# Performance work log

Hardware: AMD Instinct MI355X
Metric: run time of the kernel (lower is better)

## Reference

```python
import jax, jax.numpy as jnp
import numpy as np

B, N, E, D, R, M, L = 8, 8192, 16384, 128, 200, 20, 3


def setup_inputs() -> dict:
    key = jax.random.key(0)
    ks = jax.random.split(key, 16)
    return {
        "dists": jax.random.randint(ks[0], (B, N), 0, 10),
        "edge_index": jax.random.randint(ks[1], (B, 2, E), 0, N),
        "rels": jax.random.randint(ks[2], (B, E), 0, R),
        "node_mask": jax.random.randint(ks[3], (B, N), 0, 2).astype(bool),
        "edge_mask": jax.random.randint(ks[4], (B, E), 0, 2).astype(bool),
        "r_query_embed": jax.random.normal(ks[5], (B, D), dtype=jnp.float32),
        "conf_embeds": jax.random.normal(ks[6], (B, E, D), dtype=jnp.float32),
        "noise": jax.random.normal(ks[7], (B, N, D), dtype=jnp.float32),
        "dist_table": jax.random.normal(ks[8], (10, D), dtype=jnp.float32) * 0.02,
        "rel_table": jax.random.normal(ks[9], (R, D), dtype=jnp.float32) * 0.02,
        "msg_W": jax.random.normal(ks[10], (L, 5 * D, D), dtype=jnp.float32) / np.sqrt(5 * D),
        "msg_b": jnp.zeros((L, D), jnp.float32),
        "upd_W": jax.random.normal(ks[11], (L, D, D), dtype=jnp.float32) / np.sqrt(D),
        "upd_b": jnp.zeros((L, D), jnp.float32),
        "att_W": jax.random.normal(ks[12], (2 * D, 1), dtype=jnp.float32) / np.sqrt(2 * D),
        "att_b": jnp.zeros((1,), jnp.float32),
    }


def reference(dists, edge_index, rels, node_mask, edge_mask, r_query_embed,
              conf_embeds, noise, dist_table, rel_table, msg_W, msg_b,
              upd_W, upd_b, att_W, att_b):
    dist_emb = dist_table[jnp.clip(dists, 0, 9)]            # [B,N,D]
    h = dist_emb + noise * 0.1
    src = edge_index[:, 0, :]                               # [B,E]
    tgt = edge_index[:, 1, :]                               # [B,E]
    em = edge_mask[..., None].astype(h.dtype)               # [B,E,1]
    h_r = rel_table[rels]                                   # [B,E,D]
    dist_src = jnp.take_along_axis(dist_emb, src[..., None], axis=1)  # [B,E,D]

    def scatter_add(t_idx, msg):
        return jnp.zeros((N, D), msg.dtype).at[t_idx].add(msg)

    for k in range(L):
        h_src = jnp.take_along_axis(h, src[..., None], axis=1)        # [B,E,D]
        comp = h_src * h_r
        msg_in = jnp.concatenate([comp, h_src, dist_src, h_r, conf_embeds], axis=-1)  # [B,E,5D]
        msg = jax.nn.relu(jnp.einsum('bef,fd->bed', msg_in, msg_W[k]) + msg_b[k]) * em
        aggr = jax.vmap(scatter_add)(tgt, msg)                        # [B,N,D]
        h = jnp.einsum('bnd,df->bnf', aggr, upd_W[k]) + upd_b[k] + h

    h = h * node_mask[..., None].astype(h.dtype)
    t_state = h[:, 0, :]
    r_q = jnp.broadcast_to(r_query_embed[:, None, :], (B, N, D))
    att_in = jnp.concatenate([h, r_q], axis=-1)                       # [B,N,2D]
    scores = jax.nn.leaky_relu((att_in @ att_W + att_b)[..., 0], 0.01)
    scores = jnp.where(node_mask, scores, -1e9)
    alpha = jax.nn.softmax(scores, axis=1)
    topk_vals, topk_idx = jax.lax.top_k(alpha, M)                     # [B,M]
    H_evd = jnp.take_along_axis(h, topk_idx[..., None], axis=1) * topk_vals[..., None]
    return (H_evd, t_state)
```

## Files before the change

### kernel.cpp

```cpp
#include <hip/hip_runtime.h>
#include <hip/hip_bf16.h>
#include <math.h>

#define B_ 8
#define N_ 8192
#define E_ 16384
#define D_ 128
#define R_ 200
#define M_ 20
#define L_ 3
#define KEFF 384

typedef __attribute__((ext_vector_type(8))) short bf16x8;
typedef __attribute__((ext_vector_type(4))) float f32x4;

__device__ __forceinline__ short f2b(float f) {
  union { __hip_bfloat16 b; short s; } u;
  u.b = __float2bfloat16(f);
  return u.s;
}

__global__ __launch_bounds__(256) void k_init_h(const int* __restrict__ dists,
    const float* __restrict__ noise, const float* __restrict__ dist_table,
    float* __restrict__ h) {
  int i = blockIdx.x * 256 + threadIdx.x;
  int row = i >> 5;
  int d4 = i & 31;
  int dc = dists[row]; dc = dc < 0 ? 0 : (dc > 9 ? 9 : dc);
  const float4 t = *(const float4*)&dist_table[dc * D_ + d4 * 4];
  const float4 nz = *(const float4*)&noise[(size_t)i * 4];
  float4 o;
  o.x = t.x + 0.1f * nz.x; o.y = t.y + 0.1f * nz.y;
  o.z = t.z + 0.1f * nz.z; o.w = t.w + 0.1f * nz.w;
  *(float4*)&h[(size_t)i * 4] = o;
}

__global__ __launch_bounds__(256) void k_compact(const int* __restrict__ edge_mask,
    int* __restrict__ count, int* __restrict__ list) {
  int i = blockIdx.x * 256 + threadIdx.x;
  bool act = edge_mask[i] != 0;
  unsigned long long m = __ballot(act);
  int lane = threadIdx.x & 63;
  int base = 0;
  if (lane == 0) base = atomicAdd(count, __popcll(m));
  base = __shfl(base, 0);
  if (act) list[base + __popcll(m & ((1ull << lane) - 1ull))] = i;
}

__global__ __launch_bounds__(128) void k_tables(const float* __restrict__ dist_table,
    const float* __restrict__ rel_table, const float* __restrict__ msg_W,
    const float* __restrict__ msg_b, float* __restrict__ T3b, float* __restrict__ T4) {
  int k = blockIdx.x / 210;
  int r = blockIdx.x % 210;
  int d = threadIdx.x;
  if (r < 10) {
    float acc = msg_b[k * D_ + d];
    for (int f = 0; f < D_; ++f)
      acc = fmaf(dist_table[r * D_ + f], msg_W[(size_t)(k * 640 + 256 + f) * D_ + d], acc);
    T3b[(k * 10 + r) * D_ + d] = acc;
  } else {
    int rr = r - 10;
    float acc = 0.f;
    for (int f = 0; f < D_; ++f)
      acc = fmaf(rel_table[rr * D_ + f], msg_W[(size_t)(k * 640 + 384 + f) * D_ + d], acc);
    T4[(k * R_ + rr) * D_ + d] = acc;
  }
}

__global__ __launch_bounds__(256) void k_wbt_msg(const float* __restrict__ msg_W,
    short* __restrict__ Wbt) {
  int idx = blockIdx.x * 256 + threadIdx.x;
  int fe = idx % KEFF;
  int t = idx / KEFF;
  int n = t & 127;
  int k = t >> 7;
  int row = fe < 256 ? fe : fe + 256;
  Wbt[idx] = f2b(msg_W[(size_t)(k * 640 + row) * D_ + n]);
}

__global__ __launch_bounds__(256) void k_wbt_upd(const float* __restrict__ upd_W,
    short* __restrict__ Wbt) {
  int idx = blockIdx.x * 256 + threadIdx.x;
  int f = idx & 127;
  int t = idx >> 7;
  int n = t & 127;
  int k = t >> 7;
  Wbt[idx] = f2b(upd_W[(size_t)(k * D_ + f) * D_ + n]);
}

__global__ __launch_bounds__(256) void k_msg(
    const int* __restrict__ count_p, const int* __restrict__ list,
    const int* __restrict__ edge_index, const int* __restrict__ rels,
    const int* __restrict__ dists, const float* __restrict__ h,
    const float* __restrict__ rel_table, const float* __restrict__ conf,
    const short* __restrict__ Wbt,
    const float* __restrict__ T3b,
    const float* __restrict__ T4,
    float* __restrict__ aggr) {
  int cnt = *count_p;
  int base = blockIdx.x * 64;
  if (base >= cnt) return;
  int ne = min(64, cnt - base);
  __shared__ __align__(16) short sA[64][72];
  __shared__ __align__(16) short sB[128][72];
  __shared__ int sMeta[64][5];
  int tid = threadIdx.x;
  if (tid < 64) {
    if (tid < ne) {
      int id = list[base + tid];
      int b = id >> 14;
      int e = id & (E_ - 1);
      int src = edge_index[(b * 2) * E_ + e];
      int tgt = edge_index[(b * 2 + 1) * E_ + e];
      int dc = dists[b * N_ + src];
      dc = dc < 0 ? 0 : (dc > 9 ? 9 : dc);
      sMeta[tid][0] = b * N_ + src;
      sMeta[tid][1] = id;
      sMeta[tid][2] = b * N_ + tgt;
      sMeta[tid][3] = dc;
      sMeta[tid][4] = rels[id];
    } else {
      sMeta[tid][0] = 0; sMeta[tid][1] = 0; sMeta[tid][2] = 0;
      sMeta[tid][3] = 0; sMeta[tid][4] = 0;
    }
  }
  __syncthreads();
  int lane = tid & 63, wv = tid >> 6;
  int wm = wv >> 1, wn = wv & 1;
  int g = lane >> 4, cl = lane & 15;
  f32x4 acc[2][4];
  f32x4 zz = {0.f, 0.f, 0.f, 0.f};
#pragma unroll
  for (int tm = 0; tm < 2; ++tm)
#pragma unroll
    for (int tn = 0; tn < 4; ++tn) acc[tm][tn] = zz;
  int si = tid >> 2, sq = tid & 3;
  int nB = tid >> 1, hB = tid & 1;
  for (int kc = 0; kc < 6; ++kc) {
    float v[16];
    if (si < ne) {
      int c0 = kc * 64 + sq * 16;
      if (kc < 2) {
        const float4* hp = (const float4*)&h[(size_t)sMeta[si][0] * D_ + c0];
        const float4* rp = (const float4*)&rel_table[sMeta[si][4] * D_ + c0];
#pragma unroll
        for (int j = 0; j < 4; ++j) {
          float4 a = hp[j], r = rp[j];
          v[4*j] = a.x*r.x; v[4*j+1] = a.y*r.y; v[4*j+2] = a.z*r.z; v[4*j+3] = a.w*r.w;
        }
      } else if (kc < 4) {
        const float4* hp = (const float4*)&h[(size_t)sMeta[si][0] * D_ + (c0 - 128)];
#pragma unroll
        for (int j = 0; j < 4; ++j) {
          float4 a = hp[j];
          v[4*j] = a.x; v[4*j+1] = a.y; v[4*j+2] = a.z; v[4*j+3] = a.w;
        }
      } else {
        const float4* cp = (const float4*)&conf[(size_t)sMeta[si][1] * D_ + (c0 - 256)];
#pragma unroll
        for (int j = 0; j < 4; ++j) {
          float4 a = cp[j];
          v[4*j] = a.x; v[4*j+1] = a.y; v[4*j+2] = a.z; v[4*j+3] = a.w;
        }
      }
    } else {
#pragma unroll
      for (int j = 0; j < 16; ++j) v[j] = 0.f;
    }
    bf16x8 p0, p1;
#pragma unroll
    for (int j = 0; j < 8; ++j) { p0[j] = f2b(v[j]); p1[j] = f2b(v[j + 8]); }
    *(bf16x8*)&sA[si][sq * 16] = p0;
    *(bf16x8*)&sA[si][sq * 16 + 8] = p1;
    const bf16x8* wp = (const bf16x8*)&Wbt[(size_t)nB * KEFF + kc * 64 + hB * 32];
#pragma unroll
    for (int j = 0; j < 4; ++j) *(bf16x8*)&sB[nB][hB * 32 + j * 8] = wp[j];
    __syncthreads();
#pragma unroll
    for (int ks = 0; ks < 2; ++ks) {
      int co = ks * 32 + g * 8;
      bf16x8 af[2], bfr[4];
      af[0] = *(const bf16x8*)&sA[wm * 32 + cl][co];
      af[1] = *(const bf16x8*)&sA[wm * 32 + 16 + cl][co];
#pragma unroll
      for (int tn = 0; tn < 4; ++tn)
        bfr[tn] = *(const bf16x8*)&sB[wn * 64 + tn * 16 + cl][co];
#pragma unroll
      for (int tm = 0; tm < 2; ++tm)
#pragma unroll
        for (int tn = 0; tn < 4; ++tn)
          acc[tm][tn] = __builtin_amdgcn_mfma_f32_16x16x32_bf16(af[tm], bfr[tn], acc[tm][tn], 0, 0, 0);
    }
    __syncthreads();
  }
#pragma unroll
  for (int tm = 0; tm < 2; ++tm)
#pragma unroll
    for (int reg = 0; reg < 4; ++reg) {
      int edge = wm * 32 + tm * 16 + g * 4 + reg;
      if (edge < ne) {
        int arow = sMeta[edge][2];
        int dc = sMeta[edge][3];
        int rl = sMeta[edge][4];
#pragma unroll
        for (int tn = 0; tn < 4; ++tn) {
          int n = wn * 64 + tn * 16 + cl;
          float bias = T3b[dc * D_ + n] + T4[rl * D_ + n];
          float vv = fmaxf(acc[tm][tn][reg] + bias, 0.f);
          unsafeAtomicAdd(&aggr[(size_t)arow * D_ + n], vv);
        }
      }
    }
}

__global__ __launch_bounds__(256) void k_upd(
    float* __restrict__ aggr, const short* __restrict__ Wbt,
    const float* __restrict__ upd_b, float* __restrict__ h) {
  int base = blockIdx.x * 64;
  __shared__ __align__(16) short sA[64][72];
  __shared__ __align__(16) short sB[128][72];
  int tid = threadIdx.x;
  int lane = tid & 63, wv = tid >> 6;
  int wm = wv >> 1, wn = wv & 1;
  int g = lane >> 4, cl = lane & 15;
  f32x4 acc[2][4];
  f32x4 zz = {0.f, 0.f, 0.f, 0.f};
#pragma unroll
  for (int tm = 0; tm < 2; ++tm)
#pragma unroll
    for (int tn = 0; tn < 4; ++tn) acc[tm][tn] = zz;
  int si = tid >> 2, sq = tid & 3;
  int nB = tid >> 1, hB = tid & 1;
  for (int kc = 0; kc < 2; ++kc) {
    float4* ap = (float4*)&aggr[(size_t)(base + si) * D_ + kc * 64 + sq * 16];
    float v[16];
    float4 z4 = make_float4(0.f, 0.f, 0.f, 0.f);
#pragma unroll
    for (int j = 0; j < 4; ++j) {
      float4 a = ap[j];
      ap[j] = z4;
      v[4*j] = a.x; v[4*j+1] = a.y; v[4*j+2] = a.z; v[4*j+3] = a.w;
    }
    bf16x8 p0, p1;
#pragma unroll
    for (int j = 0; j < 8; ++j) { p0[j] = f2b(v[j]); p1[j] = f2b(v[j + 8]); }
    *(bf16x8*)&sA[si][sq * 16] = p0;
    *(bf16x8*)&sA[si][sq * 16 + 8] = p1;
    const bf16x8* wp = (const bf16x8*)&Wbt[(size_t)nB * D_ + kc * 64 + hB * 32];
#pragma unroll
    for (int j = 0; j < 4; ++j) *(bf16x8*)&sB[nB][hB * 32 + j * 8] = wp[j];
    __syncthreads();
#pragma unroll
    for (int ks = 0; ks < 2; ++ks) {
      int co = ks * 32 + g * 8;
      bf16x8 af[2], bfr[4];
      af[0] = *(const bf16x8*)&sA[wm * 32 + cl][co];
      af[1] = *(const bf16x8*)&sA[wm * 32 + 16 + cl][co];
#pragma unroll
      for (int tn = 0; tn < 4; ++tn)
        bfr[tn] = *(const bf16x8*)&sB[wn * 64 + tn * 16 + cl][co];
#pragma unroll
      for (int tm = 0; tm < 2; ++tm)
#pragma unroll
        for (int tn = 0; tn < 4; ++tn)
          acc[tm][tn] = __builtin_amdgcn_mfma_f32_16x16x32_bf16(af[tm], bfr[tn], acc[tm][tn], 0, 0, 0);
    }
    __syncthreads();
  }
#pragma unroll
  for (int tm = 0; tm < 2; ++tm)
#pragma unroll
    for (int reg = 0; reg < 4; ++reg) {
      int grow = base + wm * 32 + tm * 16 + g * 4 + reg;
#pragma unroll
      for (int tn = 0; tn < 4; ++tn) {
        int n = wn * 64 + tn * 16 + cl;
        size_t gi = (size_t)grow * D_ + n;
        h[gi] = acc[tm][tn][reg] + upd_b[n] + h[gi];
      }
    }
}

__global__ __launch_bounds__(256) void k_score(const float* __restrict__ h,
    const int* __restrict__ node_mask, const float* __restrict__ r_query,
    const float* __restrict__ att_W, const float* __restrict__ att_b,
    float* __restrict__ sSg) {
  int wv = threadIdx.x >> 6, lane = threadIdx.x & 63;
  int node = blockIdx.x * 4 + wv;
  int b = node >> 13;
  float s;
  if (node_mask[node] == 0) {
    s = -1e9f;
  } else {
    float2 hv = *(const float2*)&h[(size_t)node * D_ + lane * 2];
    float2 w0 = *(const float2*)&att_W[lane * 2];
    float2 w1 = *(const float2*)&att_W[D_ + lane * 2];
    float2 rq = *(const float2*)&r_query[b * D_ + lane * 2];
    float v = hv.x * w0.x + hv.y * w0.y + rq.x * w1.x + rq.y * w1.y;
#pragma unroll
    for (int off = 32; off > 0; off >>= 1) v += __shfl_xor(v, off);
    v += att_b[0];
    s = v > 0.f ? v : 0.01f * v;
  }
  if (lane == 0) sSg[node] = s;
}

__global__ __launch_bounds__(1024) void k_top(const float* __restrict__ sSg,
    const float* __restrict__ h, const int* __restrict__ node_mask,
    float* __restrict__ out) {
  int b = blockIdx.x;
  int tid = threadIdx.x, lane = tid & 63, wv = tid >> 6;
  __shared__ float sS[N_];
  __shared__ float sRw[16];
  __shared__ float sSegV[16];
  __shared__ int sSegI[16];
  __shared__ float sTopV[M_];
  __shared__ int sTopI[M_];
  __shared__ float sMax, sSum;
  const float4* gp = (const float4*)&sSg[(size_t)b * N_];
#pragma unroll
  for (int r = 0; r < 2; ++r) {
    float4 x = gp[tid + r * 1024];
    *(float4*)&sS[(tid + r * 1024) * 4] = x;
  }
  __syncthreads();
  float lm = -INFINITY;
  for (int n = tid; n < N_; n += 1024) lm = fmaxf(lm, sS[n]);
#pragma unroll
  for (int off = 32; off > 0; off >>= 1) lm = fmaxf(lm, __shfl_xor(lm, off));
  if (lane == 0) sRw[wv] = lm;
  __syncthreads();
  if (tid == 0) {
    float m = sRw[0];
    for (int i = 1; i < 16; ++i) m = fmaxf(m, sRw[i]);
    sMax = m;
  }
  __syncthreads();
  float mx = sMax;
  float ls = 0.f;
  for (int n = tid; n < N_; n += 1024) ls += expf(sS[n] - mx);
#pragma unroll
  for (int off = 32; off > 0; off >>= 1) ls += __shfl_xor(ls, off);
  if (lane == 0) sRw[wv] = ls;
  __syncthreads();
  if (tid == 0) {
    float s = 0.f;
    for (int i = 0; i < 16; ++i) s += sRw[i];
    sSum = s;
  }
  {
    float bv = -INFINITY; int bi = 0;
    int s0 = wv * 512;
    for (int t2 = 0; t2 < 8; ++t2) {
      int n = s0 + lane + t2 * 64;
      float x = sS[n];
      if (x > bv) { bv = x; bi = n; }
    }
#pragma unroll
    for (int off = 32; off > 0; off >>= 1) {
      float vv = __shfl_xor(bv, off); int ii = __shfl_xor(bi, off);
      if (vv > bv || (vv == bv && ii < bi)) { bv = vv; bi = ii; }
    }
    if (lane == 0) { sSegV[wv] = bv; sSegI[wv] = bi; }
  }
  __syncthreads();
  for (int j = 0; j < M_; ++j) {
    if (wv == 0) {
      float bv = (lane < 16) ? sSegV[lane] : -INFINITY;
      int bi = (lane < 16) ? sSegI[lane] : 0x7fffffff;
#pragma unroll
      for (int off = 32; off > 0; off >>= 1) {
        float vv = __shfl_xor(bv, off); int ii = __shfl_xor(bi, off);
        if (vv > bv || (vv == bv && ii < bi)) { bv = vv; bi = ii; }
      }
      if (lane == 0) { sTopV[j] = bv; sTopI[j] = bi; sS[bi] = -INFINITY; }
    }
    __syncthreads();
    int seg = sTopI[j] >> 9;
    if (wv == seg) {
      float bv = -INFINITY; int bi = 0;
      int s0 = wv * 512;
      for (int t2 = 0; t2 < 8; ++t2) {
        int n = s0 + lane + t2 * 64;
        float x = sS[n];
        if (x > bv) { bv = x; bi = n; }
      }
#pragma unroll
      for (int off = 32; off > 0; off >>= 1) {
        float vv = __shfl_xor(bv, off); int ii = __shfl_xor(bi, off);
        if (vv > bv || (vv == bv && ii < bi)) { bv = vv; bi = ii; }
      }
      if (lane == 0) { sSegV[wv] = bv; sSegI[wv] = bi; }
    }
    __syncthreads();
  }
  float sum = sSum;
  if (tid < D_) {
    float vv = node_mask[b * N_] ? h[(size_t)b * N_ * D_ + tid] : 0.f;
    out[B_ * M_ * D_ + b * D_ + tid] = vv;
  }
  for (int s2 = tid; s2 < M_ * D_; s2 += 1024) {
    int j = s2 >> 7, d = s2 & 127;
    int idx = sTopI[j];
    float alpha = expf(sTopV[j] - mx) / sum;
    float hv = h[((size_t)b * N_ + idx) * D_ + d];
    if (!node_mask[b * N_ + idx]) hv = 0.f;
    out[(b * M_ + j) * D_ + d] = hv * alpha;
  }
}

extern "C" void kernel_launch(void* const* d_in, const int* in_sizes, int n_in,
                              void* d_out, int out_size, void* d_ws, size_t ws_size,
                              hipStream_t stream) {
  const int*   dists      = (const int*)d_in[0];
  const int*   edge_index = (const int*)d_in[1];
  const int*   rels       = (const int*)d_in[2];
  const int*   node_mask  = (const int*)d_in[3];
  const int*   edge_mask  = (const int*)d_in[4];
  const float* r_query    = (const float*)d_in[5];
  const float* conf       = (const float*)d_in[6];
  const float* noise      = (const float*)d_in[7];
  const float* dist_table = (const float*)d_in[8];
  const float* rel_table  = (const float*)d_in[9];
  const float* msg_W      = (const float*)d_in[10];
  const float* msg_b      = (const float*)d_in[11];
  const float* upd_W      = (const float*)d_in[12];
  const float* upd_b      = (const float*)d_in[13];
  const float* att_W      = (const float*)d_in[14];
  const float* att_b      = (const float*)d_in[15];
  float* out = (float*)d_out;

  char* ws = (char*)d_ws;
  size_t off = 0;
  auto alloc = [&](size_t bytes) {
    void* p = ws + off;
    off = (off + bytes + 255) & ~(size_t)255;
    return p;
  };
  int*   count   = (int*)alloc(4);
  int*   list    = (int*)alloc((size_t)B_ * E_ * 4);
  float* h       = (float*)alloc((size_t)B_ * N_ * D_ * 4);
  float* aggr    = (float*)alloc((size_t)B_ * N_ * D_ * 4);
  short* Wbt_msg = (short*)alloc((size_t)L_ * D_ * KEFF * 2);
  short* Wbt_upd = (short*)alloc((size_t)L_ * D_ * D_ * 2);
  float* T3b     = (float*)alloc((size_t)L_ * 10 * D_ * 4);
  float* T4      = (float*)alloc((size_t)L_ * R_ * D_ * 4);
  float* scores  = (float*)alloc((size_t)B_ * N_ * 4);
  (void)ws_size; (void)in_sizes; (void)n_in; (void)out_size;

  hipMemsetAsync(count, 0, 4, stream);
  hipMemsetAsync(aggr, 0, (size_t)B_ * N_ * D_ * 4, stream);

  k_init_h<<<B_ * N_ * D_ / 4 / 256, 256, 0, stream>>>(dists, noise, dist_table, h);
  k_compact<<<B_ * E_ / 256, 256, 0, stream>>>(edge_mask, count, list);
  k_tables<<<L_ * 210, 128, 0, stream>>>(dist_table, rel_table, msg_W, msg_b, T3b, T4);
  k_wbt_msg<<<L_ * D_ * KEFF / 256, 256, 0, stream>>>(msg_W, Wbt_msg);
  k_wbt_upd<<<L_ * D_ * D_ / 256, 256, 0, stream>>>(upd_W, Wbt_upd);

  for (int k = 0; k < L_; ++k) {
    k_msg<<<B_ * E_ / 64, 256, 0, stream>>>(count, list, edge_index, rels, dists, h,
        rel_table, conf, Wbt_msg + (size_t)k * D_ * KEFF,
        T3b + k * 10 * D_, T4 + k * R_ * D_, aggr);
    k_upd<<<B_ * N_ / 64, 256, 0, stream>>>(aggr, Wbt_upd + (size_t)k * D_ * D_,
        upd_b + k * D_, h);
  }
  k_score<<<B_ * N_ / 4, 256, 0, stream>>>(h, node_mask, r_query, att_W, att_b, scores);
  k_top<<<B_, 1024, 0, stream>>>(scores, h, node_mask, out);
}
```

Baseline: 475.1 us.

## Load MFMA operands directly from global memory, bypassing LDS staging

Both the message and update GEMM kernels now have each lane load its A-fragment rows (gathered h, rel, conf, or aggr) and its B-fragment weights straight from global memory into registers, then convert to bf16. This removes the shared-memory tiles and the per-chunk __syncthreads barriers. The cost is redundant global loads: each row is read by two waves and each weight column by two waves, and the access pattern is less coalesced. In the update kernel, zeroing of aggr moves to after the MFMA loop behind a block barrier.

```diff
diff --git a/kernel.cpp b/kernel.cpp
--- a/kernel.cpp
+++ b/kernel.cpp
@@ -18,6 +18,18 @@
   union { __hip_bfloat16 b; short s; } u;
   u.b = __float2bfloat16(f);
   return u.s;
+}
+__device__ __forceinline__ bf16x8 pack8(float4 x, float4 y) {
+  bf16x8 r;
+  r[0] = f2b(x.x); r[1] = f2b(x.y); r[2] = f2b(x.z); r[3] = f2b(x.w);
+  r[4] = f2b(y.x); r[5] = f2b(y.y); r[6] = f2b(y.z); r[7] = f2b(y.w);
+  return r;
+}
+__device__ __forceinline__ bf16x8 pack8mul(float4 x, float4 rx, float4 y, float4 ry) {
+  bf16x8 r;
+  r[0] = f2b(x.x * rx.x); r[1] = f2b(x.y * rx.y); r[2] = f2b(x.z * rx.z); r[3] = f2b(x.w * rx.w);
+  r[4] = f2b(y.x * ry.x); r[5] = f2b(y.y * ry.y); r[6] = f2b(y.z * ry.z); r[7] = f2b(y.w * ry.w);
+  return r;
 }
 
 __global__ __launch_bounds__(256) void k_init_h(const int* __restrict__ dists,
@@ -101,97 +113,75 @@
   int base = blockIdx.x * 64;
   if (base >= cnt) return;
   int ne = min(64, cnt - base);
-  __shared__ __align__(16) short sA[64][72];
-  __shared__ __align__(16) short sB[128][72];
   __shared__ int sMeta[64][5];
   int tid = threadIdx.x;
   if (tid < 64) {
-    if (tid < ne) {
-      int id = list[base + tid];
-      int b = id >> 14;
-      int e = id & (E_ - 1);
-      int src = edge_index[(b * 2) * E_ + e];
-      int tgt = edge_index[(b * 2 + 1) * E_ + e];
-      int dc = dists[b * N_ + src];
-      dc = dc < 0 ? 0 : (dc > 9 ? 9 : dc);
-      sMeta[tid][0] = b * N_ + src;
-      sMeta[tid][1] = id;
-      sMeta[tid][2] = b * N_ + tgt;
-      sMeta[tid][3] = dc;
-      sMeta[tid][4] = rels[id];
-    } else {
-      sMeta[tid][0] = 0; sMeta[tid][1] = 0; sMeta[tid][2] = 0;
-      sMeta[tid][3] = 0; sMeta[tid][4] = 0;
-    }
+    int t = tid < ne ? tid : 0;
+    int id = list[base + t];
+    int b = id >> 14;
+    int e = id & (E_ - 1);
+    int src = edge_index[(b * 2) * E_ + e];
+    int tgt = edge_index[(b * 2 + 1) * E_ + e];
+    int dc = dists[b * N_ + src];
+    dc = dc < 0 ? 0 : (dc > 9 ? 9 : dc);
+    sMeta[tid][0] = b * N_ + src;
+    sMeta[tid][1] = id;
+    sMeta[tid][2] = b * N_ + tgt;
+    sMeta[tid][3] = dc;
+    sMeta[tid][4] = rels[id];
   }
   __syncthreads();
   int lane = tid & 63, wv = tid >> 6;
   int wm = wv >> 1, wn = wv & 1;
   int g = lane >> 4, cl = lane & 15;
+  int r0 = wm * 32 + cl, r1 = r0 + 16;
+  const float* ph0 = h + (size_t)sMeta[r0][0] * D_;
+  const float* ph1 = h + (size_t)sMeta[r1][0] * D_;
+  const float* pr0 = rel_table + (size_t)sMeta[r0][4] * D_;
+  const float* pr1 = rel_table + (size_t)sMeta[r1][4] * D_;
+  const float* pc0 = conf + (size_t)sMeta[r0][1] * D_;
+  const float* pc1 = conf + (size_t)sMeta[r1][1] * D_;
+  const short* wb = Wbt + (size_t)(wn * 64 + cl) * KEFF;
+
   f32x4 acc[2][4];
   f32x4 zz = {0.f, 0.f, 0.f, 0.f};
 #pragma unroll
   for (int tm = 0; tm < 2; ++tm)
 #pragma unroll
     for (int tn = 0; tn < 4; ++tn) acc[tm][tn] = zz;
-  int si = tid >> 2, sq = tid & 3;
-  int nB = tid >> 1, hB = tid & 1;
-  for (int kc = 0; kc < 6; ++kc) {
-    float v[16];
-    if (si < ne) {
-      int c0 = kc * 64 + sq * 16;
-      if (kc < 2) {
-        const float4* hp = (const float4*)&h[(size_t)sMeta[si][0] * D_ + c0];
-        const float4* rp = (const float4*)&rel_table[sMeta[si][4] * D_ + c0];
-#pragma unroll
-        for (int j = 0; j < 4; ++j) {
-          float4 a = hp[j], r = rp[j];
-          v[4*j] = a.x*r.x; v[4*j+1] = a.y*r.y; v[4*j+2] = a.z*r.z; v[4*j+3] = a.w*r.w;
-        }
-      } else if (kc < 4) {
-        const float4* hp = (const float4*)&h[(size_t)sMeta[si][0] * D_ + (c0 - 128)];
-#pragma unroll
-        for (int j = 0; j < 4; ++j) {
-          float4 a = hp[j];
-          v[4*j] = a.x; v[4*j+1] = a.y; v[4*j+2] = a.z; v[4*j+3] = a.w;
-        }
-      } else {
-        const float4* cp = (const float4*)&conf[(size_t)sMeta[si][1] * D_ + (c0 - 256)];
-#pragma unroll
-        for (int j = 0; j < 4; ++j) {
-          float4 a = cp[j];
-          v[4*j] = a.x; v[4*j+1] = a.y; v[4*j+2] = a.z; v[4*j+3] = a.w;
-        }
-      }
+
+#pragma unroll
+  for (int kstep = 0; kstep < 12; ++kstep) {
+    const int phase = kstep >> 2;
+    const int o = (kstep & 3) * 32 + g * 8;
+    bf16x8 a0, a1;
+    if (phase == 0) {
+      float4 xa = *(const float4*)(ph0 + o), xb = *(const float4*)(ph0 + o + 4);
+      float4 ra = *(const float4*)(pr0 + o), rb = *(const float4*)(pr0 + o + 4);
+      float4 ya = *(const float4*)(ph1 + o), yb = *(const float4*)(ph1 + o + 4);
+      float4 sa = *(const float4*)(pr1 + o), sb = *(const float4*)(pr1 + o + 4);
+      a0 = pack8mul(xa, ra, xb, rb);
+      a1 = pack8mul(ya, sa, yb, sb);
+    } else if (phase == 1) {
+      a0 = pack8(*(const float4*)(ph0 + o), *(const float4*)(ph0 + o + 4));
+      a1 = pack8(*(const float4*)(ph1 + o), *(const float4*)(ph1 + o + 4));
     } else {
-#pragma unroll
-      for (int j = 0; j < 16; ++j) v[j] = 0.f;
-    }
-    bf16x8 p0, p1;
-#pragma unroll
-    for (int j = 0; j < 8; ++j) { p0[j] = f2b(v[j]); p1[j] = f2b(v[j + 8]); }
-    *(bf16x8*)&sA[si][sq * 16] = p0;
-    *(bf16x8*)&sA[si][sq * 16 + 8] = p1;
-    const bf16x8* wp = (const bf16x8*)&Wbt[(size_t)nB * KEFF + kc * 64 + hB * 32];
-#pragma unroll
-    for (int j = 0; j < 4; ++j) *(bf16x8*)&sB[nB][hB * 32 + j * 8] = wp[j];
-    __syncthreads();
-#pragma unroll
-    for (int ks = 0; ks < 2; ++ks) {
-      int co = ks * 32 + g * 8;
-      bf16x8 af[2], bfr[4];
-      af[0] = *(const bf16x8*)&sA[wm * 32 + cl][co];
-      af[1] = *(const bf16x8*)&sA[wm * 32 + 16 + cl][co];
-#pragma unroll
-      for (int tn = 0; tn < 4; ++tn)
-        bfr[tn] = *(const bf16x8*)&sB[wn * 64 + tn * 16 + cl][co];
-#pragma unroll
-      for (int tm = 0; tm < 2; ++tm)
-#pragma unroll
-        for (int tn = 0; tn < 4; ++tn)
-          acc[tm][tn] = __builtin_amdgcn_mfma_f32_16x16x32_bf16(af[tm], bfr[tn], acc[tm][tn], 0, 0, 0);
-    }
-    __syncthreads();
+      a0 = pack8(*(const float4*)(pc0 + o), *(const float4*)(pc0 + o + 4));
+      a1 = pack8(*(const float4*)(pc1 + o), *(const float4*)(pc1 + o + 4));
+    }
+    const short* wk = wb + kstep * 32 + g * 8;
+    bf16x8 b0 = *(const bf16x8*)(wk);
+    bf16x8 b1 = *(const bf16x8*)(wk + 16 * KEFF);
+    bf16x8 b2 = *(const bf16x8*)(wk + 32 * KEFF);
+    bf16x8 b3 = *(const bf16x8*)(wk + 48 * KEFF);
+    acc[0][0] = __builtin_amdgcn_mfma_f32_16x16x32_bf16(a0, b0, acc[0][0], 0, 0, 0);
+    acc[0][1] = __builtin_amdgcn_mfma_f32_16x16x32_bf16(a0, b1, acc[0][1], 0, 0, 0);
+    acc[0][2] = __builtin_amdgcn_mfma_f32_16x16x32_bf16(a0, b2, acc[0][2], 0, 0, 0);
+    acc[0][3] = __builtin_amdgcn_mfma_f32_16x16x32_bf16(a0, b3, acc[0][3], 0, 0, 0);
+    acc[1][0] = __builtin_amdgcn_mfma_f32_16x16x32_bf16(a1, b0, acc[1][0], 0, 0, 0);
+    acc[1][1] = __builtin_amdgcn_mfma_f32_16x16x32_bf16(a1, b1, acc[1][1], 0, 0, 0);
+    acc[1][2] = __builtin_amdgcn_mfma_f32_16x16x32_bf16(a1, b2, acc[1][2], 0, 0, 0);
+    acc[1][3] = __builtin_amdgcn_mfma_f32_16x16x32_bf16(a1, b3, acc[1][3], 0, 0, 0);
   }
 #pragma unroll
   for (int tm = 0; tm < 2; ++tm)
@@ -217,56 +207,45 @@
     float* __restrict__ aggr, const short* __restrict__ Wbt,
     const float* __restrict__ upd_b, float* __restrict__ h) {
   int base = blockIdx.x * 64;
-  __shared__ __align__(16) short sA[64][72];
-  __shared__ __align__(16) short sB[128][72];
   int tid = threadIdx.x;
   int lane = tid & 63, wv = tid >> 6;
   int wm = wv >> 1, wn = wv & 1;
   int g = lane >> 4, cl = lane & 15;
+  const float* pa0 = aggr + (size_t)(base + wm * 32 + cl) * D_;
+  const float* pa1 = pa0 + 16 * D_;
+  const short* wb = Wbt + (size_t)(wn * 64 + cl) * D_;
+
   f32x4 acc[2][4];
   f32x4 zz = {0.f, 0.f, 0.f, 0.f};
 #pragma unroll
   for (int tm = 0; tm < 2; ++tm)
 #pragma unroll
     for (int tn = 0; tn < 4; ++tn) acc[tm][tn] = zz;
-  int si = tid >> 2, sq = tid & 3;
-  int nB = tid >> 1, hB = tid & 1;
-  for (int kc = 0; kc < 2; ++kc) {
-    float4* ap = (float4*)&aggr[(size_t)(base + si) * D_ + kc * 64 + sq * 16];
-    float v[16];
-    float4 z4 = make_float4(0.f, 0.f, 0.f, 0.f);
-#pragma unroll
-    for (int j = 0; j < 4; ++j) {
-      float4 a = ap[j];
-      ap[j] = z4;
-      v[4*j] = a.x; v[4*j+1] = a.y; v[4*j+2] = a.z; v[4*j+3] = a.w;
-    }
-    bf16x8 p0, p1;
-#pragma unroll
-    for (int j = 0; j < 8; ++j) { p0[j] = f2b(v[j]); p1[j] = f2b(v[j + 8]); }
-    *(bf16x8*)&sA[si][sq * 16] = p0;
-    *(bf16x8*)&sA[si][sq * 16 + 8] = p1;
-    const bf16x8* wp = (const bf16x8*)&Wbt[(size_t)nB * D_ + kc * 64 + hB * 32];
-#pragma unroll
-    for (int j = 0; j < 4; ++j) *(bf16x8*)&sB[nB][hB * 32 + j * 8] = wp[j];
-    __syncthreads();
-#pragma unroll
-    for (int ks = 0; ks < 2; ++ks) {
-      int co = ks * 32 + g * 8;
-      bf16x8 af[2], bfr[4];
-      af[0] = *(const bf16x8*)&sA[wm * 32 + cl][co];
-      af[1] = *(const bf16x8*)&sA[wm * 32 + 16 + cl][co];
-#pragma unroll
-      for (int tn = 0; tn < 4; ++tn)
-        bfr[tn] = *(const bf16x8*)&sB[wn * 64 + tn * 16 + cl][co];
-#pragma unroll
-      for (int tm = 0; tm < 2; ++tm)
-#pragma unroll
-        for (int tn = 0; tn < 4; ++tn)
-          acc[tm][tn] = __builtin_amdgcn_mfma_f32_16x16x32_bf16(af[tm], bfr[tn], acc[tm][tn], 0, 0, 0);
-    }
-    __syncthreads();
-  }
+
+#pragma unroll
+  for (int kstep = 0; kstep < 4; ++kstep) {
+    int o = kstep * 32 + g * 8;
+    bf16x8 a0 = pack8(*(const float4*)(pa0 + o), *(const float4*)(pa0 + o + 4));
+    bf16x8 a1 = pack8(*(const float4*)(pa1 + o), *(const float4*)(pa1 + o + 4));
+    const short* wk = wb + o;
+    bf16x8 b0 = *(const bf16x8*)(wk);
+    bf16x8 b1 = *(const bf16x8*)(wk + 16 * D_);
+    bf16x8 b2 = *(const bf16x8*)(wk + 32 * D_);
+    bf16x8 b3 = *(const bf16x8*)(wk + 48 * D_);
+    acc[0][0] = __builtin_amdgcn_mfma_f32_16x16x32_bf16(a0, b0, acc[0][0], 0, 0, 0);
+    acc[0][1] = __builtin_amdgcn_mfma_f32_16x16x32_bf16(a0, b1, acc[0][1], 0, 0, 0);
+    acc[0][2] = __builtin_amdgcn_mfma_f32_16x16x32_bf16(a0, b2, acc[0][2], 0, 0, 0);
+    acc[0][3] = __builtin_amdgcn_mfma_f32_16x16x32_bf16(a0, b3, acc[0][3], 0, 0, 0);
+    acc[1][0] = __builtin_amdgcn_mfma_f32_16x16x32_bf16(a1, b0, acc[1][0], 0, 0, 0);
+    acc[1][1] = __builtin_amdgcn_mfma_f32_16x16x32_bf16(a1, b1, acc[1][1], 0, 0, 0);
+    acc[1][2] = __builtin_amdgcn_mfma_f32_16x16x32_bf16(a1, b2, acc[1][2], 0, 0, 0);
+    acc[1][3] = __builtin_amdgcn_mfma_f32_16x16x32_bf16(a1, b3, acc[1][3], 0, 0, 0);
+  }
+  __syncthreads();
+  float4 z4 = make_float4(0.f, 0.f, 0.f, 0.f);
+  float4* az = (float4*)(aggr + (size_t)base * D_);
+#pragma unroll
+  for (int s = 0; s < 8; ++s) az[tid + s * 256] = z4;
 #pragma unroll
   for (int tm = 0; tm < 2; ++tm)
 #pragma unroll
```

After: 605.0 us. +27.4%, slower.
